# Optimization experiments

Measured on AMD Instinct MI355X. Metric: run time of the kernel, lower is better.

## Reference

```python
import jax, jax.numpy as jnp
import numpy as np

NQ = 5          # qubits
DIM = 2 ** NQ   # 32 amplitudes
NL = 4          # StronglyEntanglingLayers depth


def _rot_matrix(phi, theta, omega):
    """PennyLane Rot(phi,theta,omega) = RZ(omega) @ RY(theta) @ RZ(phi)."""
    c = jnp.cos(theta / 2)
    s = jnp.sin(theta / 2)
    ep = jnp.exp(-0.5j * (phi + omega).astype(jnp.complex64))
    em = jnp.exp(-0.5j * (phi - omega).astype(jnp.complex64))
    return jnp.array([[0, 0], [0, 0]], jnp.complex64).at[0, 0].set(ep * c).at[0, 1].set(-jnp.conj(em) * s).at[1, 0].set(em * s).at[1, 1].set(jnp.conj(ep) * c)


def _apply_1q(state, U, w):
    # state: (B, 2,2,2,2,2); apply 2x2 U on qubit axis w
    state = jnp.moveaxis(state, w + 1, -1)
    state = state @ U.T
    return jnp.moveaxis(state, -1, w + 1)


def _apply_cnot(state, c, t):
    # flip target axis on the control=1 slice
    s0 = jax.lax.index_in_dim(state, 0, axis=c + 1, keepdims=True)
    s1 = jax.lax.index_in_dim(state, 1, axis=c + 1, keepdims=True)
    s1 = jnp.flip(s1, axis=t + 1)
    return jnp.concatenate([s0, s1], axis=c + 1)


def setup_inputs() -> dict:
    key = jax.random.key(0)
    k1, k2 = jax.random.split(key)
    inputs = jax.random.normal(k1, (524288, 30), dtype=jnp.float32)
    weights = jax.random.normal(k2, (NL, NQ, 3), dtype=jnp.float32)
    return {"inputs": inputs, "weights": weights}


def reference(inputs, weights):
    B = inputs.shape[0]
    # AmplitudeEmbedding: pad with zeros to 32 amplitudes, normalize per sample
    padded = jnp.pad(inputs, ((0, 0), (0, DIM - inputs.shape[1])))
    norm = jnp.linalg.norm(padded, axis=1, keepdims=True)
    state = (padded / norm).astype(jnp.complex64)
    state = state.reshape((B,) + (2,) * NQ)

    # StronglyEntanglingLayers
    for l in range(NL):
        for w in range(NQ):
            U = _rot_matrix(weights[l, w, 0], weights[l, w, 1], weights[l, w, 2])
            state = _apply_1q(state, U, w)
        r = (l % (NQ - 1)) + 1  # default imprimitive range pattern
        for w in range(NQ):
            state = _apply_cnot(state, w, (w + r) % NQ)

    # expval(PauliZ(i)) for each wire
    probs = jnp.abs(state) ** 2  # (B,2,2,2,2,2)
    evs = []
    for w in range(NQ):
        axes = tuple(a for a in range(1, NQ + 1) if a != w + 1)
        p = probs.sum(axis=axes)  # (B,2)
        evs.append(p[:, 0] - p[:, 1])
    return jnp.stack(evs, axis=1)  # (B, NQ)
```

## Files before the change

### kernel.cpp

```cpp
#include <hip/hip_runtime.h>

#define NQ 5
#define DIM 32
#define NL 4
#define NFEAT 30
#define NGATES (NL * NQ)

typedef float f32x4 __attribute__((ext_vector_type(4)));
typedef float f32x2 __attribute__((ext_vector_type(2)));
typedef short bf16x8 __attribute__((ext_vector_type(8)));

static __device__ __forceinline__ unsigned short f2bf(float f) {
    unsigned u = __float_as_uint(f);
    u += 0x7FFFu + ((u >> 16) & 1u);
    return (unsigned short)(u >> 16);
}

static __device__ __forceinline__ unsigned cvt_pk_bf16(float a, float b) {
    unsigned d;
    asm("v_cvt_pk_bf16_f32 %0, %1, %2" : "=v"(d) : "v"(a), "v"(b));
    return d;
}

__global__ __launch_bounds__(128) void build_unitary(const float* __restrict__ W,
                                                     unsigned short* __restrict__ Ubf) {
    __shared__ __align__(16) float g[NGATES][8];

    const int t = threadIdx.x;
    if (t < NGATES) {
        const float phi = W[t * 3 + 0];
        const float th  = W[t * 3 + 1];
        const float om  = W[t * 3 + 2];
        const float c = cosf(0.5f * th), s = sinf(0.5f * th);
        const float a  = 0.5f * (phi + om);
        const float bb = 0.5f * (phi - om);
        const float epr = cosf(a),  epi = -sinf(a);
        const float emr = cosf(bb), emi = -sinf(bb);
        g[t][0] = epr * c;   g[t][1] = epi * c;
        g[t][2] = -emr * s;  g[t][3] = emi * s;
        g[t][4] = emr * s;   g[t][5] = emi * s;
        g[t][6] = epr * c;   g[t][7] = -epi * c;
    }
    __syncthreads();

    const int z = t & 31;
    const int j = blockIdx.x * 4 + (t >> 5);

    float ar = (z == j) ? 1.0f : 0.0f;
    float ai = 0.0f;

#pragma unroll
    for (int l = 0; l < NL; ++l) {
#pragma unroll
        for (int w = 0; w < NQ; ++w) {
            const int gi = l * NQ + w;
            const f32x4 glo = *reinterpret_cast<const f32x4*>(&g[gi][0]);
            const f32x4 ghi = *reinterpret_cast<const f32x4*>(&g[gi][4]);
            const int shift = 4 - w;
            const int msk = 1 << shift;
            const int bit = (z >> shift) & 1;
            const float pr = __shfl_xor(ar, msk, 32);
            const float pi = __shfl_xor(ai, msk, 32);
            const float csr = bit ? ghi.z : glo.x;
            const float csi = bit ? ghi.w : glo.y;
            const float cpr = bit ? ghi.x : glo.z;
            const float cpi = bit ? ghi.y : glo.w;
            const float nar = csr * ar - csi * ai + cpr * pr - cpi * pi;
            const float nai = csr * ai + csi * ar + cpr * pi + cpi * pr;
            ar = nar; ai = nai;
        }
        const int r = (l % (NQ - 1)) + 1;
#pragma unroll
        for (int cq = 0; cq < NQ; ++cq) {
            const int tq = (cq + r) % NQ;
            const int cs = 4 - cq, ts = 4 - tq;
            const int tmask = 1 << ts;
            const float pr = __shfl_xor(ar, tmask, 32);
            const float pi = __shfl_xor(ai, tmask, 32);
            const int ctrl = (z >> cs) & 1;
            ar = ctrl ? pr : ar;
            ai = ctrl ? pi : ai;
        }
    }

    Ubf[(2 * z + 0) * 32 + j] = f2bf(ar);
    Ubf[(2 * z + 1) * 32 + j] = f2bf(ai);
}

__global__ __launch_bounds__(256) void qforward(const float* __restrict__ X,
                                                const unsigned short* __restrict__ Ubf,
                                                float* __restrict__ out, int B) {
    __shared__ __align__(16) float xs[2][4 * 64 * NFEAT];
    const int tid  = threadIdx.x;
    const int lane = tid & 63;
    const int g    = lane >> 4;
    const int r    = lane & 15;
    const int wv   = tid >> 6;

    const int ntiles = (B + 255) >> 8;
    const int t0 = blockIdx.x * 4;

    bf16x8 afrag[4];
#pragma unroll
    for (int t = 0; t < 4; ++t)
        afrag[t] = *reinterpret_cast<const bf16x8*>(Ubf + (16 * t + r) * 32 + g * 8);

    const long Btot = (long)B * NFEAT;

    auto stage = [&](int tile, int buf) {
        if (tile >= ntiles) return;
        const long gbase = (long)tile * (256 * NFEAT) + wv * (64 * NFEAT);
        float* lb = &xs[buf][wv * (64 * NFEAT)];
#pragma unroll
        for (int it = 0; it < 8; ++it) {
            const int fi = it * 256 + lane * 4;
            if (fi < 64 * NFEAT && gbase + fi + 4 <= Btot)
                __builtin_amdgcn_global_load_lds(
                    (const __attribute__((address_space(1))) unsigned*)(X + gbase + fi),
                    (__attribute__((address_space(3))) unsigned*)(lb + fi),
                    16, 0, 2 );
        }
    };

    const float sg2 = (g & 2) ? -1.f : 1.f;
    const float sg3 = (g & 1) ? -1.f : 1.f;

    float oA[4][4], oB[4][4];

#define COMPUTE_TILE(I)                                                          \
    {                                                                            \
        const float* lbase = &xs[(I) & 1][wv * (64 * NFEAT)];                    \
        _Pragma("unroll")                                                        \
        for (int st = 0; st < 4; ++st) {                                         \
            const float* rowp = lbase + (st * 16 + r) * NFEAT + g * 8;           \
            f32x2 v0 = *reinterpret_cast<const f32x2*>(rowp + 0);                \
            f32x2 v1 = *reinterpret_cast<const f32x2*>(rowp + 2);                \
            f32x2 v2 = *reinterpret_cast<const f32x2*>(rowp + 4);                \
            f32x2 v3 = (g == 3) ? (f32x2){0.f, 0.f}                              \
                                : *reinterpret_cast<const f32x2*>(rowp + 6);     \
            bf16x8 bfrag;                                                        \
            unsigned* bw = reinterpret_cast<unsigned*>(&bfrag);                  \
            bw[0] = cvt_pk_bf16(v0.x, v0.y);                                     \
            bw[1] = cvt_pk_bf16(v1.x, v1.y);                                     \
            bw[2] = cvt_pk_bf16(v2.x, v2.y);                                     \
            bw[3] = cvt_pk_bf16(v3.x, v3.y);                                     \
            f32x4 d[4];                                                          \
            _Pragma("unroll")                                                    \
            for (int t = 0; t < 4; ++t)                                          \
                d[t] = __builtin_amdgcn_mfma_f32_16x16x32_bf16(                  \
                    afrag[t], bfrag, (f32x4){0.f, 0.f, 0.f, 0.f}, 0, 0, 0);      \
            float ev0 = 0.f, ev1 = 0.f, ev2 = 0.f, ev3 = 0.f, ev4 = 0.f,         \
                  nrm = 0.f;                                                     \
            _Pragma("unroll")                                                    \
            for (int t = 0; t < 4; ++t) {                                        \
                const float p0 = d[t].x * d[t].x + d[t].y * d[t].y;              \
                const float p1 = d[t].z * d[t].z + d[t].w * d[t].w;              \
                const float pt = p0 + p1;                                        \
                nrm += pt;                                                       \
                ev0 += (t & 2) ? -pt : pt;                                       \
                ev1 += (t & 1) ? -pt : pt;                                       \
                ev2 = fmaf(sg2, pt, ev2);                                        \
                ev3 = fmaf(sg3, pt, ev3);                                        \
                ev4 += p0 - p1;                                                  \
            }                                                                    \
            ev0 += __shfl_xor(ev0, 16, 64); ev0 += __shfl_xor(ev0, 32, 64);      \
            ev1 += __shfl_xor(ev1, 16, 64); ev1 += __shfl_xor(ev1, 32, 64);      \
            ev2 += __shfl_xor(ev2, 16, 64); ev2 += __shfl_xor(ev2, 32, 64);      \
            ev3 += __shfl_xor(ev3, 16, 64); ev3 += __shfl_xor(ev3, 32, 64);      \
            ev4 += __shfl_xor(ev4, 16, 64); ev4 += __shfl_xor(ev4, 32, 64);      \
            nrm += __shfl_xor(nrm, 16, 64); nrm += __shfl_xor(nrm, 32, 64);      \
            const float inv = 1.0f / nrm;                                        \
            const float mine = (g == 0) ? ev0 : (g == 1) ? ev1                   \
                             : (g == 2) ? ev2 : ev3;                             \
            oA[(I)][st] = mine * inv;                                            \
            oB[(I)][st] = ev4 * inv;                                             \
        }                                                                        \
    }

    stage(t0 + 0, 0);
    stage(t0 + 1, 1);
    asm volatile("s_waitcnt vmcnt(8)" ::: "memory");
    __builtin_amdgcn_sched_barrier(0);
    COMPUTE_TILE(0)
    asm volatile("" ::: "memory");
    stage(t0 + 2, 0);
    asm volatile("s_waitcnt vmcnt(8)" ::: "memory");
    __builtin_amdgcn_sched_barrier(0);
    COMPUTE_TILE(1)
    asm volatile("" ::: "memory");
    stage(t0 + 3, 1);
    asm volatile("s_waitcnt vmcnt(8)" ::: "memory");
    __builtin_amdgcn_sched_barrier(0);
    COMPUTE_TILE(2)
    asm volatile("s_waitcnt vmcnt(0)" ::: "memory");
    __builtin_amdgcn_sched_barrier(0);
    COMPUTE_TILE(3)
#undef COMPUTE_TILE

#pragma unroll
    for (int i = 0; i < 4; ++i) {
#pragma unroll
        for (int st = 0; st < 4; ++st) {
            const int s = (t0 + i) * 256 + wv * 64 + st * 16 + r;
            if (s < B) {
                __builtin_nontemporal_store(oA[i][st], &out[s * NQ + g]);
                if (g == 0)
                    __builtin_nontemporal_store(oB[i][st], &out[s * NQ + 4]);
            }
        }
    }
}

extern "C" void kernel_launch(void* const* d_in, const int* in_sizes, int n_in,
                              void* d_out, int out_size, void* d_ws, size_t ws_size,
                              hipStream_t stream) {
    const float* X = (const float*)d_in[0];
    const float* W = (const float*)d_in[1];
    float* out = (float*)d_out;
    const int B = in_sizes[0] / NFEAT;

    unsigned short* Ubf = (unsigned short*)d_ws;

    build_unitary<<<8, 128, 0, stream>>>(W, Ubf);

    const int ntiles = (B + 255) / 256;
    const int nblocks = (ntiles + 3) / 4;
    qforward<<<nblocks, 256, 0, stream>>>(X, Ubf, out, B);
}
```

Before: 23.62 us.

## Halve per-block tile size, raise occupancy hint, add fast full-tile path

Tiles shrink from 256 to 128 samples, so each wave handles 32 rows and LDS use per block halves. The grid doubles in block count, and launch bounds request 5 blocks per SIMD to raise occupancy for this memory-bound stream. A fast path for blocks with all four tiles valid keeps the double-buffered pipeline with adjusted waitcnt values, while tail blocks fall back to a serial load-then-compute sequence. The cost is more blocks with less work each, plus possible register pressure from the occupancy hint.

```diff
diff --git a/kernel.cpp b/kernel.cpp
--- a/kernel.cpp
+++ b/kernel.cpp
@@ -87,34 +87,34 @@
     Ubf[(2 * z + 1) * 32 + j] = f2bf(ai);
 }
 
-__global__ __launch_bounds__(256) void qforward(const float* __restrict__ X,
-                                                const unsigned short* __restrict__ Ubf,
-                                                float* __restrict__ out, int B) {
-    __shared__ __align__(16) float xs[2][4 * 64 * NFEAT];
+__global__ __launch_bounds__(256, 5) void qforward(const float* __restrict__ X,
+                                                   const unsigned short* __restrict__ Ubf,
+                                                   float* __restrict__ out, int B) {
+    __shared__ __align__(16) float xs[2][4 * 32 * NFEAT];
     const int tid  = threadIdx.x;
     const int lane = tid & 63;
     const int g    = lane >> 4;
     const int r    = lane & 15;
     const int wv   = tid >> 6;
 
-    const int ntiles = (B + 255) >> 8;
+    const int ntiles = (B + 127) >> 7;
     const int t0 = blockIdx.x * 4;
 
     bf16x8 afrag[4];
 #pragma unroll
     for (int t = 0; t < 4; ++t)
         afrag[t] = *reinterpret_cast<const bf16x8*>(Ubf + (16 * t + r) * 32 + g * 8);
+    __builtin_amdgcn_sched_barrier(0);
 
     const long Btot = (long)B * NFEAT;
 
     auto stage = [&](int tile, int buf) {
-        if (tile >= ntiles) return;
-        const long gbase = (long)tile * (256 * NFEAT) + wv * (64 * NFEAT);
-        float* lb = &xs[buf][wv * (64 * NFEAT)];
-#pragma unroll
-        for (int it = 0; it < 8; ++it) {
+        const long gbase = (long)tile * (128 * NFEAT) + wv * (32 * NFEAT);
+        float* lb = &xs[buf][wv * (32 * NFEAT)];
+#pragma unroll
+        for (int it = 0; it < 4; ++it) {
             const int fi = it * 256 + lane * 4;
-            if (fi < 64 * NFEAT && gbase + fi + 4 <= Btot)
+            if (fi < 32 * NFEAT && gbase + fi + 4 <= Btot)
                 __builtin_amdgcn_global_load_lds(
                     (const __attribute__((address_space(1))) unsigned*)(X + gbase + fi),
                     (__attribute__((address_space(3))) unsigned*)(lb + fi),
@@ -125,13 +125,13 @@
     const float sg2 = (g & 2) ? -1.f : 1.f;
     const float sg3 = (g & 1) ? -1.f : 1.f;
 
-    float oA[4][4], oB[4][4];
+    float oA[4][2], oB[4][2];
 
 #define COMPUTE_TILE(I)                                                          \
     {                                                                            \
-        const float* lbase = &xs[(I) & 1][wv * (64 * NFEAT)];                    \
+        const float* lbase = &xs[(I) & 1][wv * (32 * NFEAT)];                    \
         _Pragma("unroll")                                                        \
-        for (int st = 0; st < 4; ++st) {                                         \
+        for (int st = 0; st < 2; ++st) {                                         \
             const float* rowp = lbase + (st * 16 + r) * NFEAT + g * 8;           \
             f32x2 v0 = *reinterpret_cast<const f32x2*>(rowp + 0);                \
             f32x2 v1 = *reinterpret_cast<const f32x2*>(rowp + 2);                \
@@ -177,31 +177,58 @@
         }                                                                        \
     }
 
-    stage(t0 + 0, 0);
-    stage(t0 + 1, 1);
-    asm volatile("s_waitcnt vmcnt(8)" ::: "memory");
-    __builtin_amdgcn_sched_barrier(0);
-    COMPUTE_TILE(0)
-    asm volatile("" ::: "memory");
-    stage(t0 + 2, 0);
-    asm volatile("s_waitcnt vmcnt(8)" ::: "memory");
-    __builtin_amdgcn_sched_barrier(0);
-    COMPUTE_TILE(1)
-    asm volatile("" ::: "memory");
-    stage(t0 + 3, 1);
-    asm volatile("s_waitcnt vmcnt(8)" ::: "memory");
-    __builtin_amdgcn_sched_barrier(0);
-    COMPUTE_TILE(2)
-    asm volatile("s_waitcnt vmcnt(0)" ::: "memory");
-    __builtin_amdgcn_sched_barrier(0);
-    COMPUTE_TILE(3)
+    if (t0 + 4 <= ntiles) {
+        stage(t0 + 0, 0);
+        stage(t0 + 1, 1);
+        asm volatile("s_waitcnt vmcnt(4)" ::: "memory");
+        __builtin_amdgcn_sched_barrier(0);
+        COMPUTE_TILE(0)
+        asm volatile("" ::: "memory");
+        stage(t0 + 2, 0);
+        asm volatile("s_waitcnt vmcnt(4)" ::: "memory");
+        __builtin_amdgcn_sched_barrier(0);
+        COMPUTE_TILE(1)
+        asm volatile("" ::: "memory");
+        stage(t0 + 3, 1);
+        asm volatile("s_waitcnt vmcnt(4)" ::: "memory");
+        __builtin_amdgcn_sched_barrier(0);
+        COMPUTE_TILE(2)
+        asm volatile("s_waitcnt vmcnt(0)" ::: "memory");
+        __builtin_amdgcn_sched_barrier(0);
+        COMPUTE_TILE(3)
+    } else {
+        if (t0 + 0 < ntiles) {
+            stage(t0 + 0, 0);
+            asm volatile("s_waitcnt vmcnt(0)" ::: "memory");
+            __builtin_amdgcn_sched_barrier(0);
+            COMPUTE_TILE(0)
+        }
+        if (t0 + 1 < ntiles) {
+            stage(t0 + 1, 1);
+            asm volatile("s_waitcnt vmcnt(0)" ::: "memory");
+            __builtin_amdgcn_sched_barrier(0);
+            COMPUTE_TILE(1)
+        }
+        if (t0 + 2 < ntiles) {
+            stage(t0 + 2, 0);
+            asm volatile("s_waitcnt vmcnt(0)" ::: "memory");
+            __builtin_amdgcn_sched_barrier(0);
+            COMPUTE_TILE(2)
+        }
+        if (t0 + 3 < ntiles) {
+            stage(t0 + 3, 1);
+            asm volatile("s_waitcnt vmcnt(0)" ::: "memory");
+            __builtin_amdgcn_sched_barrier(0);
+            COMPUTE_TILE(3)
+        }
+    }
 #undef COMPUTE_TILE
 
 #pragma unroll
     for (int i = 0; i < 4; ++i) {
 #pragma unroll
-        for (int st = 0; st < 4; ++st) {
-            const int s = (t0 + i) * 256 + wv * 64 + st * 16 + r;
+        for (int st = 0; st < 2; ++st) {
+            const int s = (t0 + i) * 128 + wv * 32 + st * 16 + r;
             if (s < B) {
                 __builtin_nontemporal_store(oA[i][st], &out[s * NQ + g]);
                 if (g == 0)
@@ -223,7 +250,7 @@
 
     build_unitary<<<8, 128, 0, stream>>>(W, Ubf);
 
-    const int ntiles = (B + 255) / 256;
+    const int ntiles = (B + 127) / 128;
     const int nblocks = (ntiles + 3) / 4;
     qforward<<<nblocks, 256, 0, stream>>>(X, Ubf, out, B);
 }
```

Measured after the change: 21.95 us. 7.1% less time.
